# Kernel tuning notes

Measured on AMD Instinct MI355X. Metric: run time of the kernel, lower is better.

Reference implementation:

```python
import jax, jax.numpy as jnp
import numpy as np

GROUPS = 8
GC = 8          # group_channels = out_channels // groups
SPAN = 32
OUT = 64
EPS = 1e-5


def _bn(x, g, b, axes):
    # training-mode batch norm (biased variance), matching torch BatchNorm forward
    m = x.mean(axis=axes, keepdims=True)
    v = x.var(axis=axes, keepdims=True)
    shape = [1] * x.ndim
    shape[1] = -1
    return (x - m) / jnp.sqrt(v + EPS) * g.reshape(shape) + b.reshape(shape)


def setup_inputs() -> dict:
    key = jax.random.key(0)
    ks = jax.random.split(key, 3)
    x = jax.random.normal(ks[0], (2, 64, 32, 32, 32), dtype=jnp.float32)
    w_qkv = jax.random.normal(ks[1], (2 * OUT, 64), dtype=jnp.float32) * 0.1
    rel_emb = jax.random.normal(ks[2], (2 * GC, 2 * SPAN - 1), dtype=jnp.float32)
    return {
        "x": x,
        "w_qkv": w_qkv,
        "bn_qkv_g": jnp.ones((2 * OUT,), jnp.float32),
        "bn_qkv_b": jnp.zeros((2 * OUT,), jnp.float32),
        "bn_sim_g": jnp.ones((3 * GROUPS,), jnp.float32),
        "bn_sim_b": jnp.zeros((3 * GROUPS,), jnp.float32),
        "bn_out_g": jnp.ones((2 * OUT,), jnp.float32),
        "bn_out_b": jnp.zeros((2 * OUT,), jnp.float32),
        "rel_emb": rel_emb,
    }


def reference(x, w_qkv, bn_qkv_g, bn_qkv_b, bn_sim_g, bn_sim_b, bn_out_g, bn_out_b, rel_emb):
    B, C, H, W, D = x.shape  # dim == 2 -> attend over depth
    L = D  # == SPAN
    xp = jnp.transpose(x, (0, 2, 3, 1, 4)).reshape(B * H * W, C, L)  # (N,C,L)
    N = xp.shape[0]

    # 1x1 conv + BatchNorm1d
    qkv = jnp.einsum('oc,ncl->nol', w_qkv, xp)
    qkv = _bn(qkv, bn_qkv_g, bn_qkv_b, axes=(0, 2))

    qkv = qkv.reshape(N, GROUPS, 2 * GC, L)
    q = qkv[:, :, : GC // 2]                # (N,g,gc/2,L)
    k = qkv[:, :, GC // 2: GC]
    v = qkv[:, :, GC:]                      # (N,g,gc,L)

    # relative embeddings -> (2*gc, span, span)
    idx = (jnp.arange(SPAN)[:, None] - jnp.arange(SPAN)[None, :] + SPAN - 1).reshape(-1)
    emb = rel_emb[:, idx].reshape(2 * GC, SPAN, SPAN)
    qe_emb = emb[: GC // 2]
    ke_emb = emb[GC // 2: GC]
    ve_emb = emb[GC:]

    qe = jnp.einsum('ngci,cij->ngij', q, qe_emb)   # (N,g,L,L)
    ke = jnp.einsum('ngci,cij->ngij', k, ke_emb)
    qk = jnp.einsum('ngci,ngcj->ngij', qe, ke)     # contracts over first L axis (faithful)

    sim = jnp.concatenate([qk, qe, ke], axis=1)    # (N,3g,L,L)
    sim = _bn(sim, bn_sim_g, bn_sim_b, axes=(0, 2, 3))
    sim = sim.reshape(N, 3, GROUPS, L, L).sum(axis=1)
    sim = jax.nn.softmax(sim, axis=3)

    am = jnp.einsum('ngij,ngcj->ngci', sim, v)       # (N,g,gc,L)
    ame = jnp.einsum('ngij,cij->ngci', sim, ve_emb)  # (N,g,gc,L)

    out = jnp.concatenate([am, ame], axis=-1).reshape(N, 2 * OUT, L)
    out = _bn(out, bn_out_g, bn_out_b, axes=(0, 2))
    out = out.reshape(B, H, W, OUT, 2, L).sum(axis=-2)   # (B,H,W,out,L)
    out = jnp.transpose(out, (0, 3, 1, 2, 4))            # (B,out,H,W,D)
    return out
```

## Files before the change

kernel.cpp:

```cpp
#include <hip/hip_runtime.h>


typedef _Float16 f16;
typedef __attribute__((ext_vector_type(2))) _Float16 f16x2;
typedef __attribute__((ext_vector_type(8))) _Float16 f16x8;
typedef __attribute__((ext_vector_type(16))) float f32x16;

struct U4 { unsigned a[4]; };
union F8 { unsigned u[4]; f16x8 v; };

__device__ __forceinline__ U4 ld4(const unsigned* p) {
    uint4 v = *(const uint4*)p;
    U4 r; r.a[0] = v.x; r.a[1] = v.y; r.a[2] = v.z; r.a[3] = v.w;
    return r;
}
__device__ __forceinline__ f16x2 u2h(unsigned u) { return __builtin_bit_cast(f16x2, u); }

__device__ __forceinline__ float fdot2u(unsigned a, unsigned b, float c) {
#if __has_builtin(__builtin_amdgcn_fdot2)
    return __builtin_amdgcn_fdot2(u2h(a), u2h(b), c, false);
#else
    f16x2 x = u2h(a), y = u2h(b);
    return (float)x.x * (float)y.x + (float)x.y * (float)y.y + c;
#endif
}
__device__ __forceinline__ unsigned pkrtz(float a, float b) {
#if __has_builtin(__builtin_amdgcn_cvt_pkrtz)
    return __builtin_bit_cast(unsigned, __builtin_amdgcn_cvt_pkrtz(a, b));
#else
    f16x2 v; v.x = (f16)a; v.y = (f16)b;
    return __builtin_bit_cast(unsigned, v);
#endif
}
__device__ __forceinline__ unsigned pkmul(unsigned a, unsigned b) {
    f16x2 x = u2h(a), y = u2h(b);
    f16x2 r = x * y;
    return __builtin_bit_cast(unsigned, r);
}

__device__ __forceinline__ float sum16(float v) {
    int x;
    x = __builtin_amdgcn_update_dpp(0, __float_as_int(v), 0x121, 0xF, 0xF, true); v += __int_as_float(x);
    x = __builtin_amdgcn_update_dpp(0, __float_as_int(v), 0x122, 0xF, 0xF, true); v += __int_as_float(x);
    x = __builtin_amdgcn_update_dpp(0, __float_as_int(v), 0x124, 0xF, 0xF, true); v += __int_as_float(x);
    x = __builtin_amdgcn_update_dpp(0, __float_as_int(v), 0x128, 0xF, 0xF, true); v += __int_as_float(x);
    return v;
}
__device__ __forceinline__ float sum32(float v) {
    v = sum16(v); return v + __shfl_xor(v, 16);
}
__device__ __forceinline__ float sum64(float v) {
    v = sum16(v); v += __shfl_xor(v, 16); return v + __shfl_xor(v, 32);
}

__global__ __launch_bounds__(256) void k_qkv(const float* __restrict__ x,
                                             const float* __restrict__ w,
                                             f16* __restrict__ qkv,
                                             float* __restrict__ pq) {
    __shared__ __attribute__((aligned(16))) unsigned xt[32 * 66];
    int t = threadIdx.x, wv = t >> 6, l = t & 63;
    int li = l & 31, h = l >> 5;
    int bid = blockIdx.x;
    int b = bid >> 9;
    int col0 = (bid & 511) * 64;
    const float* xb = x + (size_t)b * 2097152 + col0;
    #pragma unroll
    for (int k = 0; k < 4; ++k) {
        int idx = t + 256 * k;
        int col2 = idx & 31, p = idx >> 5;
        const float* r0 = xb + (size_t)(2 * p) * 32768 + 2 * col2;
        float2 a = *(const float2*)r0;
        float2 bb = *(const float2*)(r0 + 32768);
        int ks = p >> 3, hh = (p >> 1) & 1, m = (p & 1) + 2 * ((p >> 2) & 1);
        unsigned w0 = pkrtz(a.x, bb.x);
        unsigned w1 = pkrtz(a.y, bb.y);
        *(uint2*)&xt[(ks * 8 + hh * 4 + m) * 66 + 2 * col2] = make_uint2(w0, w1);
    }
    f16x8 aw[4];
    {
        const float* wr = w + (size_t)(32 * wv + li) * 64;
        #pragma unroll
        for (int ks = 0; ks < 4; ++ks) {
            float4 w0 = *(const float4*)(wr + 16 * ks + 4 * h);
            float4 w1 = *(const float4*)(wr + 16 * ks + 8 + 4 * h);
            F8 fa;
            fa.u[0] = pkrtz(w0.x, w0.y); fa.u[1] = pkrtz(w0.z, w0.w);
            fa.u[2] = pkrtz(w1.x, w1.y); fa.u[3] = pkrtz(w1.z, w1.w);
            aw[ks] = fa.v;
        }
    }
    __syncthreads();
    float s1a[16] = {}, s2a[16] = {};
    #pragma unroll
    for (int ct = 0; ct < 2; ++ct) {
        f32x16 D = {};
        #pragma unroll
        for (int ks = 0; ks < 4; ++ks) {
            F8 fb;
            #pragma unroll
            for (int m = 0; m < 4; ++m)
                fb.u[m] = xt[(ks * 8 + h * 4 + m) * 66 + ct * 32 + li];
            D = __builtin_amdgcn_mfma_f32_32x32x16_f16(aw[ks], fb.v, D, 0, 0, 0);
        }
        int colg = col0 + ct * 32 + li;
        f16* qn = qkv + (size_t)b * 4194304 + colg;
        #pragma unroll
        for (int r = 0; r < 16; ++r) {
            int och = 32 * wv + (r & 3) + 8 * (r >> 2) + 4 * h;
            qn[(size_t)och * 32768] = (f16)D[r];
            s1a[r] += D[r];
            s2a[r] += D[r] * D[r];
        }
    }
    #pragma unroll
    for (int r = 0; r < 16; ++r) {
        float s1 = sum32(s1a[r]);
        float s2 = sum32(s2a[r]);
        if (li == 0) {
            int och = 32 * wv + (r & 3) + 8 * (r >> 2) + 4 * h;
            pq[(size_t)bid * 256 + och * 2] = s1;
            pq[(size_t)bid * 256 + och * 2 + 1] = s2;
        }
    }
}

__global__ __launch_bounds__(256) void red_qkv(const float* __restrict__ pq,
                                               float* __restrict__ sqkv,
                                               const float* __restrict__ rel,
                                               f16* __restrict__ gemb) {
    int t = threadIdx.x;
    int base = blockIdx.x * 64;
    float acc = 0;
    #pragma unroll 8
    for (int k = 0; k < 64; ++k) acc += pq[(size_t)(base + k) * 256 + t];
    atomicAdd(&sqkv[((t & 1) ? 128 : 0) + (t >> 1)], acc);
    int tid = blockIdx.x * 256 + t;
    for (int e = tid; e < 4608; e += 4096) {
        int c2 = e / 1152, rm = e % 1152, y = rm / 36, x = rm % 36;
        f16 v0 = (f16)0, v1 = (f16)0;
        if (x < 32) {
            v0 = (f16)rel[(2 * c2) * 63 + x - y + 31];
            v1 = (f16)rel[(2 * c2 + 1) * 63 + x - y + 31];
        }
        gemb[2 * e] = v0; gemb[2 * e + 1] = v1;
    }
    for (int e = tid; e < 4608; e += 4096) {
        int c2 = e / 1152, rm = e % 1152, a = rm / 36, b = rm % 36;
        f16 v0 = (f16)0, v1 = (f16)0;
        if (b < 32) {
            v0 = (f16)rel[(2 * c2) * 63 + a - b + 31];
            v1 = (f16)rel[(2 * c2 + 1) * 63 + a - b + 31];
        }
        gemb[9216 + 2 * e] = v0; gemb[9216 + 2 * e + 1] = v1;
    }
    for (int e = tid; e < 9216; e += 4096) {
        int c = e / 1152, rm = e % 1152, a = rm / 36, b = rm % 36;
        gemb[18432 + e] = (b < 32) ? (f16)rel[(8 + c) * 63 + a - b + 31] : (f16)0;
    }
}

__global__ __launch_bounds__(512, 2) void k_sim(const f16* __restrict__ qkv,
                                                const f16* __restrict__ gemb,
                                                const float* __restrict__ sqkv,
                                                const float* __restrict__ bqg,
                                                const float* __restrict__ bqb,
                                                float* __restrict__ psim) {
    __shared__ __attribute__((aligned(16))) f16 qkh[2][8][256];
    __shared__ float statw[8][6];
    int t = threadIdx.x, wv = t >> 6, l = t & 63;
    int g = blockIdx.x & 7, nb = blockIdx.x >> 3;
    int li = l & 31, h = l >> 5;
    const unsigned* eT2u = (const unsigned*)gemb;
    {
        int ch = l >> 3, i0 = (l & 7) * 4;
        int cc = g * 16 + ch;
        float mu = sqkv[cc] * (1.0f / 65536.0f);
        float var = sqkv[128 + cc] * (1.0f / 65536.0f) - mu * mu;
        float aa = bqg[cc] * rsqrtf(var + 1e-5f);
        float bb = bqb[cc] - mu * aa;
        #pragma unroll
        for (int pr = 0; pr < 2; ++pr) {
            int n = nb * 8 + wv + pr * 1024;
            int b_ = n >> 10, hw = n & 1023;
            const f16* qn = qkv + (size_t)b_ * 4194304 + (size_t)(g * 16) * 32768 + hw * 32;
            uint2 q2 = *(const uint2*)(qn + (size_t)ch * 32768 + i0);
            f16x2 p0 = u2h(q2.x), p1 = u2h(q2.y);
            qkh[pr][wv][(i0 + 0) * 8 + ch] = (f16)(aa * (float)p0.x + bb);
            qkh[pr][wv][(i0 + 1) * 8 + ch] = (f16)(aa * (float)p0.y + bb);
            qkh[pr][wv][(i0 + 2) * 8 + ch] = (f16)(aa * (float)p1.x + bb);
            qkh[pr][wv][(i0 + 3) * 8 + ch] = (f16)(aa * (float)p1.y + bb);
        }
    }
    __syncthreads();
    unsigned uq[2][2][4], uk[2][2][4];
    float sqe = 0, sqe2 = 0, ske = 0, ske2 = 0;
    #pragma unroll
    for (int s = 0; s < 2; ++s) {
        #pragma unroll
        for (int blk = 0; blk < 2; ++blk) {
            int p0 = 16 * s + 4 * h + 8 * blk;
            U4 e0 = ld4(eT2u + 0 * 1152 + li * 36 + p0);
            U4 e1 = ld4(eT2u + 1 * 1152 + li * 36 + p0);
            U4 e2 = ld4(eT2u + 2 * 1152 + li * 36 + p0);
            U4 e3 = ld4(eT2u + 3 * 1152 + li * 36 + p0);
            #pragma unroll
            for (int pr = 0; pr < 2; ++pr) {
                float qe[4], ke[4];
                #pragma unroll
                for (int e = 0; e < 4; ++e) {
                    U4 qr = ld4((const unsigned*)&qkh[pr][wv][(p0 + e) * 8]);
                    qe[e] = fdot2u(qr.a[0], e0.a[e], fdot2u(qr.a[1], e1.a[e], 0.f));
                    ke[e] = fdot2u(qr.a[2], e2.a[e], fdot2u(qr.a[3], e3.a[e], 0.f));
                    sqe += qe[e]; sqe2 += qe[e] * qe[e];
                    ske += ke[e]; ske2 += ke[e] * ke[e];
                }
                uq[pr][s][2 * blk + 0] = pkrtz(qe[0], qe[1]);
                uq[pr][s][2 * blk + 1] = pkrtz(qe[2], qe[3]);
                uk[pr][s][2 * blk + 0] = pkrtz(ke[0], ke[1]);
                uk[pr][s][2 * blk + 1] = pkrtz(ke[2], ke[3]);
            }
        }
    }
    float s1 = 0, s2 = 0;
    #pragma unroll
    for (int pr = 0; pr < 2; ++pr) {
        F8 fq0, fq1, fk0, fk1;
        #pragma unroll
        for (int j = 0; j < 4; ++j) {
            fq0.u[j] = uq[pr][0][j]; fq1.u[j] = uq[pr][1][j];
            fk0.u[j] = uk[pr][0][j]; fk1.u[j] = uk[pr][1][j];
        }
        f32x16 D = {};
        D = __builtin_amdgcn_mfma_f32_32x32x16_f16(fk0.v, fq0.v, D, 0, 0, 0);
        D = __builtin_amdgcn_mfma_f32_32x32x16_f16(fk1.v, fq1.v, D, 0, 0, 0);
        #pragma unroll
        for (int r = 0; r < 16; ++r) { s1 += D[r]; s2 += D[r] * D[r]; }
    }
    s1 = sum64(s1);   s2 = sum64(s2);
    sqe = sum64(sqe); sqe2 = sum64(sqe2);
    ske = sum64(ske); ske2 = sum64(ske2);
    if (l == 0) {
        statw[wv][0] = s1;  statw[wv][1] = s2;
        statw[wv][2] = sqe; statw[wv][3] = sqe2;
        statw[wv][4] = ske; statw[wv][5] = ske2;
    }
    __syncthreads();
    if (t < 6) {
        float tot = 0;
        #pragma unroll
        for (int w2 = 0; w2 < 8; ++w2) tot += statw[w2][t];
        psim[blockIdx.x * 8 + t] = tot;
    }
}

__global__ __launch_bounds__(64) void red_sim(const float* __restrict__ psim,
                                              float* __restrict__ ssim) {
    int t = threadIdx.x;
    if (t >= 48) return;
    int g = t / 6, s = t % 6;
    float acc = 0;
    #pragma unroll 8
    for (int nb = 0; nb < 128; ++nb) acc += psim[(nb * 8 + g) * 8 + s];
    const int base[6] = {0, 24, 8, 32, 16, 40};
    ssim[base[s] + g] = acc;
}

__global__ __launch_bounds__(256, 4) void k_attn(const f16* __restrict__ qkv,
                                                 const f16* __restrict__ gemb,
                                                 const float* __restrict__ sqkv,
                                                 const float* __restrict__ bqg,
                                                 const float* __restrict__ bqb,
                                                 const float* __restrict__ ssim,
                                                 const float* __restrict__ bsg,
                                                 const float* __restrict__ bsb,
                                                 f16* __restrict__ oraw,
                                                 float* __restrict__ sout) {
    __shared__ __attribute__((aligned(16))) f16 qkh[2][4][256];
    __shared__ __attribute__((aligned(16))) f16 vh[2][4][288];
    __shared__ float statw[4][32];
    int t = threadIdx.x, wv = t >> 6, l = t & 63;
    int g = blockIdx.x & 7, nb = blockIdx.x >> 3;
    int li = l & 31, h = l >> 5;
    const unsigned* eT2u = (const unsigned*)gemb;
    const unsigned* eP2u = eT2u + 4608;
    const f16* ePvh = gemb + 18432;
    int n0 = nb * 4 + wv, n1 = n0 + 1024;
    float aQK, aQE, aKE, csum;
    {
        float m0 = ssim[g] * (1.0f / 2097152.0f);
        float v0 = ssim[24 + g] * (1.0f / 2097152.0f) - m0 * m0;
        aQK = bsg[g] * rsqrtf(v0 + 1e-5f);
        float b0 = bsb[g] - m0 * aQK;
        float m1 = ssim[8 + g] * (1.0f / 2097152.0f);
        float v1 = ssim[32 + g] * (1.0f / 2097152.0f) - m1 * m1;
        aQE = bsg[8 + g] * rsqrtf(v1 + 1e-5f);
        float b1 = bsb[8 + g] - m1 * aQE;
        float m2 = ssim[16 + g] * (1.0f / 2097152.0f);
        float v2 = ssim[40 + g] * (1.0f / 2097152.0f) - m2 * m2;
        aKE = bsg[16 + g] * rsqrtf(v2 + 1e-5f);
        float b2 = bsb[16 + g] - m2 * aKE;
        csum = b0 + b1 + b2 - 6.0f;
    }
    {
        int ch = l >> 3, i0 = (l & 7) * 4;
        int cc = g * 16 + ch;
        float mu = sqkv[cc] * (1.0f / 65536.0f);
        float var = sqkv[128 + cc] * (1.0f / 65536.0f) - mu * mu;
        float aa = bqg[cc] * rsqrtf(var + 1e-5f);
        float bb = bqb[cc] - mu * aa;
        int cv = g * 16 + 8 + ch;
        float muv = sqkv[cv] * (1.0f / 65536.0f);
        float varv = sqkv[128 + cv] * (1.0f / 65536.0f) - muv * muv;
        float av = bqg[cv] * rsqrtf(varv + 1e-5f);
        float bv = bqb[cv] - muv * av;
        #pragma unroll
        for (int pr = 0; pr < 2; ++pr) {
            int n = pr ? n1 : n0;
            int b_ = n >> 10, hw = n & 1023;
            const f16* qn = qkv + (size_t)b_ * 4194304 + (size_t)(g * 16) * 32768 + hw * 32;
            uint2 q2 = *(const uint2*)(qn + (size_t)ch * 32768 + i0);
            f16x2 p0 = u2h(q2.x), p1 = u2h(q2.y);
            qkh[pr][wv][(i0 + 0) * 8 + ch] = (f16)(aa * (float)p0.x + bb);
            qkh[pr][wv][(i0 + 1) * 8 + ch] = (f16)(aa * (float)p0.y + bb);
            qkh[pr][wv][(i0 + 2) * 8 + ch] = (f16)(aa * (float)p1.x + bb);
            qkh[pr][wv][(i0 + 3) * 8 + ch] = (f16)(aa * (float)p1.y + bb);
            uint2 v2q = *(const uint2*)(qn + (size_t)(8 + ch) * 32768 + i0);
            f16x2 v0 = u2h(v2q.x), v1q = u2h(v2q.y);
            vh[pr][wv][ch * 36 + i0 + 0] = (f16)(av * (float)v0.x + bv);
            vh[pr][wv][ch * 36 + i0 + 1] = (f16)(av * (float)v0.y + bv);
            vh[pr][wv][ch * 36 + i0 + 2] = (f16)(av * (float)v1q.x + bv);
            vh[pr][wv][ch * 36 + i0 + 3] = (f16)(av * (float)v1q.y + bv);
        }
    }
    __syncthreads();
    unsigned uq[2][2][4], uk[2][2][4];
    #pragma unroll
    for (int s = 0; s < 2; ++s) {
        #pragma unroll
        for (int blk = 0; blk < 2; ++blk) {
            int p0 = 16 * s + 4 * h + 8 * blk;
            U4 e0 = ld4(eT2u + 0 * 1152 + li * 36 + p0);
            U4 e1 = ld4(eT2u + 1 * 1152 + li * 36 + p0);
            U4 e2 = ld4(eT2u + 2 * 1152 + li * 36 + p0);
            U4 e3 = ld4(eT2u + 3 * 1152 + li * 36 + p0);
            #pragma unroll
            for (int pr = 0; pr < 2; ++pr) {
                float qe[4], ke[4];
                #pragma unroll
                for (int e = 0; e < 4; ++e) {
                    U4 qr = ld4((const unsigned*)&qkh[pr][wv][(p0 + e) * 8]);
                    qe[e] = fdot2u(qr.a[0], e0.a[e], fdot2u(qr.a[1], e1.a[e], 0.f));
                    ke[e] = fdot2u(qr.a[2], e2.a[e], fdot2u(qr.a[3], e3.a[e], 0.f));
                }
                uq[pr][s][2 * blk + 0] = pkrtz(qe[0], qe[1]);
                uq[pr][s][2 * blk + 1] = pkrtz(qe[2], qe[3]);
                uk[pr][s][2 * blk + 0] = pkrtz(ke[0], ke[1]);
                uk[pr][s][2 * blk + 1] = pkrtz(ke[2], ke[3]);
            }
        }
    }
    f32x16 Dq0 = {}, Dq1 = {};
    {
        F8 fq0, fq1, fk0, fk1;
        #pragma unroll
        for (int j = 0; j < 4; ++j) {
            fq0.u[j] = uq[0][0][j]; fq1.u[j] = uq[0][1][j];
            fk0.u[j] = uk[0][0][j]; fk1.u[j] = uk[0][1][j];
        }
        Dq0 = __builtin_amdgcn_mfma_f32_32x32x16_f16(fk0.v, fq0.v, Dq0, 0, 0, 0);
        Dq0 = __builtin_amdgcn_mfma_f32_32x32x16_f16(fk1.v, fq1.v, Dq0, 0, 0, 0);
        #pragma unroll
        for (int j = 0; j < 4; ++j) {
            fq0.u[j] = uq[1][0][j]; fq1.u[j] = uq[1][1][j];
            fk0.u[j] = uk[1][0][j]; fk1.u[j] = uk[1][1][j];
        }
        Dq1 = __builtin_amdgcn_mfma_f32_32x32x16_f16(fk0.v, fq0.v, Dq1, 0, 0, 0);
        Dq1 = __builtin_amdgcn_mfma_f32_32x32x16_f16(fk1.v, fq1.v, Dq1, 0, 0, 0);
    }
    U4 qhv0 = ld4((const unsigned*)&qkh[0][wv][li * 8]);
    U4 qhv1 = ld4((const unsigned*)&qkh[1][wv][li * 8]);
    unsigned up0[8], up1[8];
    float se0 = 0, se1 = 0;
    const unsigned one2 = 0x3C003C00u;
    #pragma unroll
    for (int rq = 0; rq < 4; ++rq) {
        int j0 = 8 * rq + 4 * h;
        U4 a0 = ld4(eP2u + 0 * 1152 + li * 36 + j0);
        U4 a1 = ld4(eP2u + 1 * 1152 + li * 36 + j0);
        U4 a2 = ld4(eP2u + 2 * 1152 + li * 36 + j0);
        U4 a3 = ld4(eP2u + 3 * 1152 + li * 36 + j0);
        float ev0[4], ev1[4];
        #pragma unroll
        for (int e = 0; e < 4; ++e) {
            float qe4 = fdot2u(qhv0.a[0], a0.a[e], fdot2u(qhv0.a[1], a1.a[e], 0.f));
            float ke4 = fdot2u(qhv0.a[2], a2.a[e], fdot2u(qhv0.a[3], a3.a[e], 0.f));
            ev0[e] = __expf(aQK * Dq0[4 * rq + e] + aQE * qe4 + aKE * ke4 + csum);
            qe4 = fdot2u(qhv1.a[0], a0.a[e], fdot2u(qhv1.a[1], a1.a[e], 0.f));
            ke4 = fdot2u(qhv1.a[2], a2.a[e], fdot2u(qhv1.a[3], a3.a[e], 0.f));
            ev1[e] = __expf(aQK * Dq1[4 * rq + e] + aQE * qe4 + aKE * ke4 + csum);
        }
        up0[2 * rq] = pkrtz(ev0[0], ev0[1]); up0[2 * rq + 1] = pkrtz(ev0[2], ev0[3]);
        up1[2 * rq] = pkrtz(ev1[0], ev1[1]); up1[2 * rq + 1] = pkrtz(ev1[2], ev1[3]);
        se0 = fdot2u(up0[2 * rq], one2, se0); se0 = fdot2u(up0[2 * rq + 1], one2, se0);
        se1 = fdot2u(up1[2 * rq], one2, se1); se1 = fdot2u(up1[2 * rq + 1], one2, se1);
    }
    se0 += __shfl_xor(se0, 32);
    se1 += __shfl_xor(se1, 32);
    float iv0 = __frcp_rn(se0), iv1 = __frcp_rn(se1);
    unsigned hi0 = pkrtz(iv0, iv0), hi1 = pkrtz(iv1, iv1);
    #pragma unroll
    for (int w2 = 0; w2 < 8; ++w2) { up0[w2] = pkmul(up0[w2], hi0); up1[w2] = pkmul(up1[w2], hi1); }
    f32x16 D20 = {}, D21 = {};
    #pragma unroll
    for (int pr = 0; pr < 2; ++pr) {
        F8 fp0, fp1, fv0, fv1;
        const unsigned* up = pr ? up1 : up0;
        fp0.u[0] = up[0]; fp0.u[1] = up[1]; fp0.u[2] = up[2]; fp0.u[3] = up[3];
        fp1.u[0] = up[4]; fp1.u[1] = up[5]; fp1.u[2] = up[6]; fp1.u[3] = up[7];
        const f16* vb = &vh[pr][wv][(li & 7) * 36];
        uint2 va0 = *(const uint2*)(vb + 4 * h);
        uint2 vb0 = *(const uint2*)(vb + 4 * h + 8);
        uint2 va1 = *(const uint2*)(vb + 16 + 4 * h);
        uint2 vb1 = *(const uint2*)(vb + 16 + 4 * h + 8);
        if (li >= 8) {
            va0 = make_uint2(0, 0); vb0 = make_uint2(0, 0);
            va1 = make_uint2(0, 0); vb1 = make_uint2(0, 0);
        }
        fv0.u[0] = va0.x; fv0.u[1] = va0.y; fv0.u[2] = vb0.x; fv0.u[3] = vb0.y;
        fv1.u[0] = va1.x; fv1.u[1] = va1.y; fv1.u[2] = vb1.x; fv1.u[3] = vb1.y;
        if (pr == 0) {
            D20 = __builtin_amdgcn_mfma_f32_32x32x16_f16(fv0.v, fp0.v, D20, 0, 0, 0);
            D20 = __builtin_amdgcn_mfma_f32_32x32x16_f16(fv1.v, fp1.v, D20, 0, 0, 0);
        } else {
            D21 = __builtin_amdgcn_mfma_f32_32x32x16_f16(fv0.v, fp0.v, D21, 0, 0, 0);
            D21 = __builtin_amdgcn_mfma_f32_32x32x16_f16(fv1.v, fp1.v, D21, 0, 0, 0);
        }
    }
    float ame0[8], ame1[8];
    #pragma unroll
    for (int c = 0; c < 8; ++c) {
        const f16* er = ePvh + (c * 32 + li) * 36;
        float a0c = 0, a1c = 0;
        #pragma unroll
        for (int s = 0; s < 2; ++s) {
            #pragma unroll
            for (int dd = 0; dd < 2; ++dd) {
                uint2 ev = *(const uint2*)(er + 16 * s + 8 * dd + 4 * h);
                int widx = 4 * s + 2 * dd;
                a0c = fdot2u(up0[widx], ev.x, a0c);
                a0c = fdot2u(up0[widx + 1], ev.y, a0c);
                a1c = fdot2u(up1[widx], ev.x, a1c);
                a1c = fdot2u(up1[widx + 1], ev.y, a1c);
            }
        }
        ame0[c] = a0c + __shfl_xor(a0c, 32);
        ame1[c] = a1c + __shfl_xor(a1c, 32);
    }
    f16* on0 = oraw + (size_t)n0 * 4096 + g * 512;
    f16* on1 = oraw + (size_t)n1 * 4096 + g * 512;
    #pragma unroll
    for (int e = 0; e < 4; ++e) {
        int c = e + 4 * h;
        float av0 = D20[e], av1 = D21[e];
        float ae0 = ame0[c], ae1 = ame1[c];
        on0[(2 * c) * 32 + li] = (f16)av0;
        on0[(2 * c + 1) * 32 + li] = (f16)ae0;
        on1[(2 * c) * 32 + li] = (f16)av1;
        on1[(2 * c + 1) * 32 + li] = (f16)ae1;
        float x1 = sum32(av0 + av1), x2 = sum32(av0 * av0 + av1 * av1);
        float y1 = sum32(ae0 + ae1), y2 = sum32(ae0 * ae0 + ae1 * ae1);
        if (li == 0) {
            statw[wv][(2 * c) * 2 + 0] = x1;     statw[wv][(2 * c) * 2 + 1] = x2;
            statw[wv][(2 * c + 1) * 2 + 0] = y1; statw[wv][(2 * c + 1) * 2 + 1] = y2;
        }
    }
    __syncthreads();
    if (t < 32) {
        float tot = statw[0][t] + statw[1][t] + statw[2][t] + statw[3][t];
        int u = t >> 1;
        int och = g * 16 + u;
        atomicAdd(&sout[((t & 1) ? 128 : 0) + och], tot);
    }
}

__global__ __launch_bounds__(256) void k_out(const f16* __restrict__ oraw,
                                             const float* __restrict__ sout,
                                             const float* __restrict__ bog,
                                             const float* __restrict__ bob,
                                             float* __restrict__ out) {
    int gid = blockIdx.x * 256 + threadIdx.x;
    int l4 = gid & 7;
    int rest = gid >> 3;
    int w2 = rest & 31; rest >>= 5;
    int hh = rest & 31; rest >>= 5;
    int oc = rest & 63;
    int b = rest >> 6;
    int n = b * 1024 + hh * 32 + w2;
    int c0 = 2 * oc, c1 = 2 * oc + 1;
    float mu0 = sout[c0] * (1.0f / 65536.0f);
    float v0 = sout[128 + c0] * (1.0f / 65536.0f) - mu0 * mu0;
    float a0 = bog[c0] * rsqrtf(v0 + 1e-5f);
    float b0 = bob[c0] - mu0 * a0;
    float mu1 = sout[c1] * (1.0f / 65536.0f);
    float v1 = sout[128 + c1] * (1.0f / 65536.0f) - mu1 * mu1;
    float a1 = bog[c1] * rsqrtf(v1 + 1e-5f);
    float b1 = bob[c1] - mu1 * a1;
    float cc = b0 + b1;
    const f16* on = oraw + (size_t)n * 4096;
    uint2 r0 = *(const uint2*)(on + oc * 64 + l4 * 4);
    uint2 r1 = *(const uint2*)(on + oc * 64 + 32 + l4 * 4);
    f16x2 r0a = u2h(r0.x), r0b = u2h(r0.y);
    f16x2 r1a = u2h(r1.x), r1b = u2h(r1.y);
    float4 o;
    o.x = a0 * (float)r0a.x + a1 * (float)r1a.x + cc;
    o.y = a0 * (float)r0a.y + a1 * (float)r1a.y + cc;
    o.z = a0 * (float)r0b.x + a1 * (float)r1b.x + cc;
    o.w = a0 * (float)r0b.y + a1 * (float)r1b.y + cc;
    *((float4*)out + gid) = o;
}

extern "C" void kernel_launch(void* const* d_in, const int* in_sizes, int n_in,
                              void* d_out, int out_size, void* d_ws, size_t ws_size,
                              hipStream_t stream) {
    const float* x   = (const float*)d_in[0];
    const float* w   = (const float*)d_in[1];
    const float* bqg = (const float*)d_in[2];
    const float* bqb = (const float*)d_in[3];
    const float* bsg = (const float*)d_in[4];
    const float* bsb = (const float*)d_in[5];
    const float* bog = (const float*)d_in[6];
    const float* bob = (const float*)d_in[7];
    const float* rel = (const float*)d_in[8];

    f16* qkv16  = (f16*)d_ws;
    f16* oraw16 = qkv16 + 8388608;
    f16* gemb   = oraw16 + 8388608;
    float* stats = (float*)(gemb + 27648);
    float* sqkv = stats;
    float* ssim = stats + 256;
    float* sout = stats + 304;
    float* pq   = stats + 576;
    float* psim = (float*)oraw16;

    hipMemsetAsync(stats, 0, 560 * sizeof(float), stream);

    k_qkv<<<1024, 256, 0, stream>>>(x, w, qkv16, pq);
    red_qkv<<<16, 256, 0, stream>>>(pq, sqkv, rel, gemb);
    k_sim<<<1024, 512, 0, stream>>>(qkv16, gemb, sqkv, bqg, bqb, psim);
    red_sim<<<1, 64, 0, stream>>>(psim, ssim);
    k_attn<<<2048, 256, 0, stream>>>(qkv16, gemb, sqkv, bqg, bqb, ssim, bsg, bsb, oraw16, sout);
    k_out<<<4096, 256, 0, stream>>>(oraw16, sout, bog, bob, (float*)d_out);
}
```

Baseline: 95.98 us.

## Process four sequences per wave in attention kernel to amortize embedding loads

Each wave in k_attn now handles four rows (n, n+512, n+1024, n+1536) instead of two, and the grid is halved. Relative-embedding loads, BN coefficient setup and the stats reduction/atomics are shared across more rows. The QK MFMA results are packed to fp16 so register pressure stays bounded, at the cost of extra rounding, higher register use and lower occupancy from more shared memory per block.

```diff
diff --git a/kernel.cpp b/kernel.cpp
--- a/kernel.cpp
+++ b/kernel.cpp
@@ -275,8 +275,8 @@
                                                  const float* __restrict__ bsb,
                                                  f16* __restrict__ oraw,
                                                  float* __restrict__ sout) {
-    __shared__ __attribute__((aligned(16))) f16 qkh[2][4][256];
-    __shared__ __attribute__((aligned(16))) f16 vh[2][4][288];
+    __shared__ __attribute__((aligned(16))) f16 qkh[4][4][256];
+    __shared__ __attribute__((aligned(16))) f16 vh[4][4][288];
     __shared__ float statw[4][32];
     int t = threadIdx.x, wv = t >> 6, l = t & 63;
     int g = blockIdx.x & 7, nb = blockIdx.x >> 3;
@@ -284,7 +284,7 @@
     const unsigned* eT2u = (const unsigned*)gemb;
     const unsigned* eP2u = eT2u + 4608;
     const f16* ePvh = gemb + 18432;
-    int n0 = nb * 4 + wv, n1 = n0 + 1024;
+    int nbase = nb * 4 + wv;
     float aQK, aQE, aKE, csum;
     {
         float m0 = ssim[g] * (1.0f / 2097152.0f);
@@ -314,8 +314,8 @@
         float av = bqg[cv] * rsqrtf(varv + 1e-5f);
         float bv = bqb[cv] - muv * av;
         #pragma unroll
-        for (int pr = 0; pr < 2; ++pr) {
-            int n = pr ? n1 : n0;
+        for (int pr = 0; pr < 4; ++pr) {
+            int n = nbase + pr * 512;
             int b_ = n >> 10, hw = n & 1023;
             const f16* qn = qkv + (size_t)b_ * 4194304 + (size_t)(g * 16) * 32768 + hw * 32;
             uint2 q2 = *(const uint2*)(qn + (size_t)ch * 32768 + i0);
@@ -333,54 +333,60 @@
         }
     }
     __syncthreads();
-    unsigned uq[2][2][4], uk[2][2][4];
-    #pragma unroll
-    for (int s = 0; s < 2; ++s) {
-        #pragma unroll
-        for (int blk = 0; blk < 2; ++blk) {
-            int p0 = 16 * s + 4 * h + 8 * blk;
-            U4 e0 = ld4(eT2u + 0 * 1152 + li * 36 + p0);
-            U4 e1 = ld4(eT2u + 1 * 1152 + li * 36 + p0);
-            U4 e2 = ld4(eT2u + 2 * 1152 + li * 36 + p0);
-            U4 e3 = ld4(eT2u + 3 * 1152 + li * 36 + p0);
-            #pragma unroll
-            for (int pr = 0; pr < 2; ++pr) {
-                float qe[4], ke[4];
+    unsigned dqp[4][8];
+    #pragma unroll
+    for (int grp = 0; grp < 2; ++grp) {
+        unsigned uq[2][2][4], uk[2][2][4];
+        #pragma unroll
+        for (int s = 0; s < 2; ++s) {
+            #pragma unroll
+            for (int blk = 0; blk < 2; ++blk) {
+                int p0 = 16 * s + 4 * h + 8 * blk;
+                U4 e0 = ld4(eT2u + 0 * 1152 + li * 36 + p0);
+                U4 e1 = ld4(eT2u + 1 * 1152 + li * 36 + p0);
+                U4 e2 = ld4(eT2u + 2 * 1152 + li * 36 + p0);
+                U4 e3 = ld4(eT2u + 3 * 1152 + li * 36 + p0);
                 #pragma unroll
-                for (int e = 0; e < 4; ++e) {
-                    U4 qr = ld4((const unsigned*)&qkh[pr][wv][(p0 + e) * 8]);
-                    qe[e] = fdot2u(qr.a[0], e0.a[e], fdot2u(qr.a[1], e1.a[e], 0.f));
-                    ke[e] = fdot2u(qr.a[2], e2.a[e], fdot2u(qr.a[3], e3.a[e], 0.f));
+                for (int pi = 0; pi < 2; ++pi) {
+                    int pr = 2 * grp + pi;
+                    float qe[4], ke[4];
+                    #pragma unroll
+                    for (int e = 0; e < 4; ++e) {
+                        U4 qr = ld4((const unsigned*)&qkh[pr][wv][(p0 + e) * 8]);
+                        qe[e] = fdot2u(qr.a[0], e0.a[e], fdot2u(qr.a[1], e1.a[e], 0.f));
+                        ke[e] = fdot2u(qr.a[2], e2.a[e], fdot2u(qr.a[3], e3.a[e], 0.f));
+                    }
+                    uq[pi][s][2 * blk + 0] = pkrtz(qe[0], qe[1]);
+                    uq[pi][s][2 * blk + 1] = pkrtz(qe[2], qe[3]);
+                    uk[pi][s][2 * blk + 0] = pkrtz(ke[0], ke[1]);
+                    uk[pi][s][2 * blk + 1] = pkrtz(ke[2], ke[3]);
                 }
-                uq[pr][s][2 * blk + 0] = pkrtz(qe[0], qe[1]);
-                uq[pr][s][2 * blk + 1] = pkrtz(qe[2], qe[3]);
-                uk[pr][s][2 * blk + 0] = pkrtz(ke[0], ke[1]);
-                uk[pr][s][2 * blk + 1] = pkrtz(ke[2], ke[3]);
             }
         }
-    }
-    f32x16 Dq0 = {}, Dq1 = {};
-    {
-        F8 fq0, fq1, fk0, fk1;
-        #pragma unroll
-        for (int j = 0; j < 4; ++j) {
-            fq0.u[j] = uq[0][0][j]; fq1.u[j] = uq[0][1][j];
-            fk0.u[j] = uk[0][0][j]; fk1.u[j] = uk[0][1][j];
-        }
-        Dq0 = __builtin_amdgcn_mfma_f32_32x32x16_f16(fk0.v, fq0.v, Dq0, 0, 0, 0);
-        Dq0 = __builtin_amdgcn_mfma_f32_32x32x16_f16(fk1.v, fq1.v, Dq0, 0, 0, 0);
-        #pragma unroll
-        for (int j = 0; j < 4; ++j) {
-            fq0.u[j] = uq[1][0][j]; fq1.u[j] = uq[1][1][j];
-            fk0.u[j] = uk[1][0][j]; fk1.u[j] = uk[1][1][j];
-        }
-        Dq1 = __builtin_amdgcn_mfma_f32_32x32x16_f16(fk0.v, fq0.v, Dq1, 0, 0, 0);
-        Dq1 = __builtin_amdgcn_mfma_f32_32x32x16_f16(fk1.v, fq1.v, Dq1, 0, 0, 0);
-    }
-    U4 qhv0 = ld4((const unsigned*)&qkh[0][wv][li * 8]);
-    U4 qhv1 = ld4((const unsigned*)&qkh[1][wv][li * 8]);
-    unsigned up0[8], up1[8];
-    float se0 = 0, se1 = 0;
+        #pragma unroll
+        for (int pi = 0; pi < 2; ++pi) {
+            int pr = 2 * grp + pi;
+            F8 fq0, fq1, fk0, fk1;
+            #pragma unroll
+            for (int j = 0; j < 4; ++j) {
+                fq0.u[j] = uq[pi][0][j]; fq1.u[j] = uq[pi][1][j];
+                fk0.u[j] = uk[pi][0][j]; fk1.u[j] = uk[pi][1][j];
+            }
+            f32x16 D = {};
+            D = __builtin_amdgcn_mfma_f32_32x32x16_f16(fk0.v, fq0.v, D, 0, 0, 0);
+            D = __builtin_amdgcn_mfma_f32_32x32x16_f16(fk1.v, fq1.v, D, 0, 0, 0);
+            #pragma unroll
+            for (int rq = 0; rq < 4; ++rq) {
+                dqp[pr][2 * rq + 0] = pkrtz(D[4 * rq + 0], D[4 * rq + 1]);
+                dqp[pr][2 * rq + 1] = pkrtz(D[4 * rq + 2], D[4 * rq + 3]);
+            }
+        }
+    }
+    U4 qhv[4];
+    #pragma unroll
+    for (int pr = 0; pr < 4; ++pr) qhv[pr] = ld4((const unsigned*)&qkh[pr][wv][li * 8]);
+    unsigned up[4][8];
+    float se[4] = {};
     const unsigned one2 = 0x3C003C00u;
     #pragma unroll
     for (int rq = 0; rq < 4; ++rq) {
@@ -389,34 +395,37 @@
         U4 a1 = ld4(eP2u + 1 * 1152 + li * 36 + j0);
         U4 a2 = ld4(eP2u + 2 * 1152 + li * 36 + j0);
         U4 a3 = ld4(eP2u + 3 * 1152 + li * 36 + j0);
-        float ev0[4], ev1[4];
-        #pragma unroll
-        for (int e = 0; e < 4; ++e) {
-            float qe4 = fdot2u(qhv0.a[0], a0.a[e], fdot2u(qhv0.a[1], a1.a[e], 0.f));
-            float ke4 = fdot2u(qhv0.a[2], a2.a[e], fdot2u(qhv0.a[3], a3.a[e], 0.f));
-            ev0[e] = __expf(aQK * Dq0[4 * rq + e] + aQE * qe4 + aKE * ke4 + csum);
-            qe4 = fdot2u(qhv1.a[0], a0.a[e], fdot2u(qhv1.a[1], a1.a[e], 0.f));
-            ke4 = fdot2u(qhv1.a[2], a2.a[e], fdot2u(qhv1.a[3], a3.a[e], 0.f));
-            ev1[e] = __expf(aQK * Dq1[4 * rq + e] + aQE * qe4 + aKE * ke4 + csum);
-        }
-        up0[2 * rq] = pkrtz(ev0[0], ev0[1]); up0[2 * rq + 1] = pkrtz(ev0[2], ev0[3]);
-        up1[2 * rq] = pkrtz(ev1[0], ev1[1]); up1[2 * rq + 1] = pkrtz(ev1[2], ev1[3]);
-        se0 = fdot2u(up0[2 * rq], one2, se0); se0 = fdot2u(up0[2 * rq + 1], one2, se0);
-        se1 = fdot2u(up1[2 * rq], one2, se1); se1 = fdot2u(up1[2 * rq + 1], one2, se1);
-    }
-    se0 += __shfl_xor(se0, 32);
-    se1 += __shfl_xor(se1, 32);
-    float iv0 = __frcp_rn(se0), iv1 = __frcp_rn(se1);
-    unsigned hi0 = pkrtz(iv0, iv0), hi1 = pkrtz(iv1, iv1);
-    #pragma unroll
-    for (int w2 = 0; w2 < 8; ++w2) { up0[w2] = pkmul(up0[w2], hi0); up1[w2] = pkmul(up1[w2], hi1); }
-    f32x16 D20 = {}, D21 = {};
-    #pragma unroll
-    for (int pr = 0; pr < 2; ++pr) {
+        #pragma unroll
+        for (int pr = 0; pr < 4; ++pr) {
+            f16x2 da = u2h(dqp[pr][2 * rq]), db = u2h(dqp[pr][2 * rq + 1]);
+            float qkv4[4] = {(float)da.x, (float)da.y, (float)db.x, (float)db.y};
+            float ev[4];
+            #pragma unroll
+            for (int e = 0; e < 4; ++e) {
+                float qe4 = fdot2u(qhv[pr].a[0], a0.a[e], fdot2u(qhv[pr].a[1], a1.a[e], 0.f));
+                float ke4 = fdot2u(qhv[pr].a[2], a2.a[e], fdot2u(qhv[pr].a[3], a3.a[e], 0.f));
+                ev[e] = __expf(aQK * qkv4[e] + aQE * qe4 + aKE * ke4 + csum);
+            }
+            up[pr][2 * rq] = pkrtz(ev[0], ev[1]);
+            up[pr][2 * rq + 1] = pkrtz(ev[2], ev[3]);
+            se[pr] = fdot2u(up[pr][2 * rq], one2, se[pr]);
+            se[pr] = fdot2u(up[pr][2 * rq + 1], one2, se[pr]);
+        }
+    }
+    #pragma unroll
+    for (int pr = 0; pr < 4; ++pr) {
+        float s = se[pr] + __shfl_xor(se[pr], 32);
+        float iv = __frcp_rn(s);
+        unsigned hiv = pkrtz(iv, iv);
+        #pragma unroll
+        for (int w2 = 0; w2 < 8; ++w2) up[pr][w2] = pkmul(up[pr][w2], hiv);
+    }
+    float avr[4][4];
+    #pragma unroll
+    for (int pr = 0; pr < 4; ++pr) {
         F8 fp0, fp1, fv0, fv1;
-        const unsigned* up = pr ? up1 : up0;
-        fp0.u[0] = up[0]; fp0.u[1] = up[1]; fp0.u[2] = up[2]; fp0.u[3] = up[3];
-        fp1.u[0] = up[4]; fp1.u[1] = up[5]; fp1.u[2] = up[6]; fp1.u[3] = up[7];
+        fp0.u[0] = up[pr][0]; fp0.u[1] = up[pr][1]; fp0.u[2] = up[pr][2]; fp0.u[3] = up[pr][3];
+        fp1.u[0] = up[pr][4]; fp1.u[1] = up[pr][5]; fp1.u[2] = up[pr][6]; fp1.u[3] = up[pr][7];
         const f16* vb = &vh[pr][wv][(li & 7) * 36];
         uint2 va0 = *(const uint2*)(vb + 4 * h);
         uint2 vb0 = *(const uint2*)(vb + 4 * h + 8);
@@ -428,47 +437,53 @@
         }
         fv0.u[0] = va0.x; fv0.u[1] = va0.y; fv0.u[2] = vb0.x; fv0.u[3] = vb0.y;
         fv1.u[0] = va1.x; fv1.u[1] = va1.y; fv1.u[2] = vb1.x; fv1.u[3] = vb1.y;
-        if (pr == 0) {
-            D20 = __builtin_amdgcn_mfma_f32_32x32x16_f16(fv0.v, fp0.v, D20, 0, 0, 0);
-            D20 = __builtin_amdgcn_mfma_f32_32x32x16_f16(fv1.v, fp1.v, D20, 0, 0, 0);
-        } else {
-            D21 = __builtin_amdgcn_mfma_f32_32x32x16_f16(fv0.v, fp0.v, D21, 0, 0, 0);
-            D21 = __builtin_amdgcn_mfma_f32_32x32x16_f16(fv1.v, fp1.v, D21, 0, 0, 0);
-        }
-    }
-    float ame0[8], ame1[8];
+        f32x16 D2 = {};
+        D2 = __builtin_amdgcn_mfma_f32_32x32x16_f16(fv0.v, fp0.v, D2, 0, 0, 0);
+        D2 = __builtin_amdgcn_mfma_f32_32x32x16_f16(fv1.v, fp1.v, D2, 0, 0, 0);
+        avr[pr][0] = D2[0]; avr[pr][1] = D2[1]; avr[pr][2] = D2[2]; avr[pr][3] = D2[3];
+    }
+    float ame[4][8];
     #pragma unroll
     for (int c = 0; c < 8; ++c) {
         const f16* er = ePvh + (c * 32 + li) * 36;
-        float a0c = 0, a1c = 0;
+        float ac[4] = {};
         #pragma unroll
         for (int s = 0; s < 2; ++s) {
             #pragma unroll
             for (int dd = 0; dd < 2; ++dd) {
                 uint2 ev = *(const uint2*)(er + 16 * s + 8 * dd + 4 * h);
                 int widx = 4 * s + 2 * dd;
-                a0c = fdot2u(up0[widx], ev.x, a0c);
-                a0c = fdot2u(up0[widx + 1], ev.y, a0c);
-                a1c = fdot2u(up1[widx], ev.x, a1c);
-                a1c = fdot2u(up1[widx + 1], ev.y, a1c);
+                #pragma unroll
+                for (int pr = 0; pr < 4; ++pr) {
+                    ac[pr] = fdot2u(up[pr][widx], ev.x, ac[pr]);
+                    ac[pr] = fdot2u(up[pr][widx + 1], ev.y, ac[pr]);
+                }
             }
         }
-        ame0[c] = a0c + __shfl_xor(a0c, 32);
-        ame1[c] = a1c + __shfl_xor(a1c, 32);
-    }
-    f16* on0 = oraw + (size_t)n0 * 4096 + g * 512;
-    f16* on1 = oraw + (size_t)n1 * 4096 + g * 512;
+        #pragma unroll
+        for (int pr = 0; pr < 4; ++pr) ame[pr][c] = ac[pr] + __shfl_xor(ac[pr], 32);
+    }
+    float osx1[4] = {}, osx2[4] = {}, osy1[4] = {}, osy2[4] = {};
+    #pragma unroll
+    for (int pr = 0; pr < 4; ++pr) {
+        int n = nbase + pr * 512;
+        f16* on = oraw + (size_t)n * 4096 + g * 512;
+        #pragma unroll
+        for (int e = 0; e < 4; ++e) {
+            int c = e + 4 * h;
+            float av = avr[pr][e];
+            float ae = ame[pr][c];
+            on[(2 * c) * 32 + li] = (f16)av;
+            on[(2 * c + 1) * 32 + li] = (f16)ae;
+            osx1[e] += av; osx2[e] += av * av;
+            osy1[e] += ae; osy2[e] += ae * ae;
+        }
+    }
     #pragma unroll
     for (int e = 0; e < 4; ++e) {
         int c = e + 4 * h;
-        float av0 = D20[e], av1 = D21[e];
-        float ae0 = ame0[c], ae1 = ame1[c];
-        on0[(2 * c) * 32 + li] = (f16)av0;
-        on0[(2 * c + 1) * 32 + li] = (f16)ae0;
-        on1[(2 * c) * 32 + li] = (f16)av1;
-        on1[(2 * c + 1) * 32 + li] = (f16)ae1;
-        float x1 = sum32(av0 + av1), x2 = sum32(av0 * av0 + av1 * av1);
-        float y1 = sum32(ae0 + ae1), y2 = sum32(ae0 * ae0 + ae1 * ae1);
+        float x1 = sum32(osx1[e]), x2 = sum32(osx2[e]);
+        float y1 = sum32(osy1[e]), y2 = sum32(osy2[e]);
         if (li == 0) {
             statw[wv][(2 * c) * 2 + 0] = x1;     statw[wv][(2 * c) * 2 + 1] = x2;
             statw[wv][(2 * c + 1) * 2 + 0] = y1; statw[wv][(2 * c + 1) * 2 + 1] = y2;
@@ -548,6 +563,6 @@
     red_qkv<<<16, 256, 0, stream>>>(pq, sqkv, rel, gemb);
     k_sim<<<1024, 512, 0, stream>>>(qkv16, gemb, sqkv, bqg, bqb, psim);
     red_sim<<<1, 64, 0, stream>>>(psim, ssim);
-    k_attn<<<2048, 256, 0, stream>>>(qkv16, gemb, sqkv, bqg, bqb, ssim, bsg, bsb, oraw16, sout);
+    k_attn<<<1024, 256, 0, stream>>>(qkv16, gemb, sqkv, bqg, bqb, ssim, bsg, bsb, oraw16, sout);
     k_out<<<4096, 256, 0, stream>>>(oraw16, sout, bog, bob, (float*)d_out);
 }
```

Result: slower. 106.8 us (+11.3%).
